# Performance work log

Measured on AMD Instinct MI355X. Metric: run time of the kernel, lower is better.

## Reference

```python
import jax, jax.numpy as jnp
import numpy as np

S, B, V, E, H, L, HM = 256, 16, 20000, 512, 256, 2, 128  # seq, batch, vocab, emb, hidden, layers, mlp hidden
THRESH = 0.5


def setup_inputs() -> dict:
    key = jax.random.key(0)
    ks = jax.random.split(key, 8)
    sc = 0.05
    concepts = jax.random.randint(ks[0], (S, B), 0, V)
    concepts_lengths = jnp.full((B,), S, dtype=jnp.int32)  # full-length sequences
    emb = jax.random.normal(ks[1], (V, E), jnp.float32) * sc
    # stacked PyTorch-style LSTM weights: [layer, direction(0=fwd,1=bwd), 4H, in]
    w_ih = jax.random.normal(ks[2], (L, 2, 4 * H, E), jnp.float32) * sc
    w_hh = jax.random.normal(ks[3], (L, 2, 4 * H, H), jnp.float32) * sc
    b = jax.random.normal(ks[4], (L, 2, 4 * H), jnp.float32) * sc  # b_ih + b_hh combined
    Ua = jax.random.normal(ks[5], (HM, 2 * H), jnp.float32) * sc
    Wa = jax.random.normal(ks[6], (HM, 2 * H), jnp.float32) * sc
    va = jax.random.normal(ks[7], (1, HM), jnp.float32) * sc
    return dict(concepts=concepts, concepts_lengths=concepts_lengths, emb=emb,
                w_ih=w_ih, w_hh=w_hh, b=b, Ua=Ua, Wa=Wa, va=va)


def _lstm_dir(x, wi, wh, bb, reverse):
    # x: [S, B, in]; PyTorch gate order i, f, g, o
    h0 = jnp.zeros((x.shape[1], H), x.dtype)

    def step(carry, xt):
        h, c = carry
        g = xt @ wi.T + h @ wh.T + bb  # [B, 4H]
        i, f, gg, o = jnp.split(g, 4, axis=-1)
        c = jax.nn.sigmoid(f) * c + jax.nn.sigmoid(i) * jnp.tanh(gg)
        h = jax.nn.sigmoid(o) * jnp.tanh(c)
        return (h, c), h

    _, hs = jax.lax.scan(step, (h0, h0), x, reverse=reverse)
    return hs  # [S, B, H]


def reference(concepts, concepts_lengths, emb, w_ih, w_hh, b, Ua, Wa, va):
    x = emb[concepts]  # [S, B, E]
    for l in range(L):  # fixed small layer count
        f = _lstm_dir(x, w_ih[l, 0], w_hh[l, 0], b[l, 0], False)
        r = _lstm_dir(x, w_ih[l, 1], w_hh[l, 1], b[l, 1], True)
        x = jnp.concatenate([f, r], axis=-1)  # [S, B, 2H]
    enc = x.transpose(1, 0, 2)  # [B, S, 2H]
    p = enc @ Ua.T  # [B, S, HM]  Ua(parent)
    c = enc @ Wa.T  # [B, S, HM]  Wa(child)
    # fused pairwise: va(tanh(Ua(p_i) + Wa(c_j))) -> [B, S, S]
    scores = jnp.einsum('bijh,h->bij', jnp.tanh(p[:, :, None, :] + c[:, None, :, :]), va[0])
    predictions = (jax.nn.sigmoid(scores) >= THRESH).astype(jnp.int32)
    return scores, predictions
```

## Files before the change

kernel.cpp:

```cpp
#include <hip/hip_runtime.h>


#define S_    256
#define B_    16
#define E_    512
#define H_    256
#define HM_   128
#define M_    4096

typedef __attribute__((ext_vector_type(8))) short short8;
typedef __attribute__((ext_vector_type(4))) float f32x4;
union u32x4s8 { unsigned int u[4]; uint4 u4; short8 v; };

__device__ __forceinline__ float sigm(float x) { return 1.f / (1.f + __expf(-x)); }
__device__ __forceinline__ float tanh_fast(float x) {
  x = fminf(fmaxf(x, -15.f), 15.f);
  float e = __expf(2.f * x);
  return (e - 1.f) / (e + 1.f);
}
__device__ __forceinline__ unsigned short f2bf(float f) {
  unsigned u = __float_as_uint(f);
  u += 0x7FFFu + ((u >> 16) & 1u);
  return (unsigned short)(u >> 16);
}
__device__ __forceinline__ float bf2f(unsigned short s) {
  return __uint_as_float(((unsigned)s) << 16);
}
__device__ __forceinline__ unsigned int packsplit(float f) {
  unsigned short m = f2bf(f);
  unsigned short r = f2bf(f - bf2f(m));
  return (unsigned)m | ((unsigned)r << 16);
}

__global__ void k_gather_pk(const int* __restrict__ concepts, const float* __restrict__ emb,
                            unsigned int* __restrict__ Xpk,
                            unsigned long long* __restrict__ hbz) {
  if (threadIdx.x < 8)
    hbz[(size_t)blockIdx.x * 8 + threadIdx.x] = 0ull;
  int m = blockIdx.x;
  int tok = concepts[m];
  const float4* src = reinterpret_cast<const float4*>(emb + (size_t)tok * E_);
  uint4* dst = reinterpret_cast<uint4*>(Xpk + (size_t)m * E_);
  for (int i = threadIdx.x; i < E_ / 4; i += blockDim.x) {
    float4 v = src[i];
    uint4 o;
    o.x = packsplit(v.x); o.y = packsplit(v.y); o.z = packsplit(v.z); o.w = packsplit(v.w);
    dst[i] = o;
  }
}

__global__ void k_pack(const float* __restrict__ in, unsigned int* __restrict__ out, int n4) {
  int i = blockIdx.x * blockDim.x + threadIdx.x;
  if (i < n4) {
    float4 v = reinterpret_cast<const float4*>(in)[i];
    uint4 o;
    o.x = packsplit(v.x); o.y = packsplit(v.y); o.z = packsplit(v.z); o.w = packsplit(v.w);
    reinterpret_cast<uint4*>(out)[i] = o;
  }
}

__global__ __launch_bounds__(256) void k_gemm_pk(const unsigned int* __restrict__ Apk,
                                                 const unsigned int* __restrict__ Wpk,
                                                 const float* __restrict__ bias,
                                                 float* __restrict__ C, int N, int K) {
  __shared__ unsigned int As[128][36];
  __shared__ unsigned int Ws2[128][36];
  const int bm = blockIdx.x * 128, bn = blockIdx.y * 128;
  const int tid = threadIdx.x;
  const int wave = tid >> 6, lane = tid & 63;
  const int wm = (wave >> 1) << 6, wn = (wave & 1) << 6;
  const int l16 = lane & 15, quad = lane >> 4;
  const int r = tid >> 1, cb = (tid & 1) << 4;

  f32x4 acc[4][4];
#pragma unroll
  for (int i = 0; i < 4; ++i)
#pragma unroll
    for (int j = 0; j < 4; ++j) acc[i][j] = (f32x4){0.f, 0.f, 0.f, 0.f};

  for (int k0 = 0; k0 < K; k0 += 32) {
    const unsigned int* pa = Apk + (size_t)(bm + r) * K + k0 + cb;
    const unsigned int* pw = Wpk + (size_t)(bn + r) * K + k0 + cb;
    uint4 a0 = *(const uint4*)pa, a1 = *(const uint4*)(pa + 4),
          a2 = *(const uint4*)(pa + 8), a3 = *(const uint4*)(pa + 12);
    uint4 w0 = *(const uint4*)pw, w1 = *(const uint4*)(pw + 4),
          w2 = *(const uint4*)(pw + 8), w3 = *(const uint4*)(pw + 12);
    __syncthreads();
    *(uint4*)&As[r][cb] = a0;  *(uint4*)&As[r][cb + 4] = a1;
    *(uint4*)&As[r][cb + 8] = a2; *(uint4*)&As[r][cb + 12] = a3;
    *(uint4*)&Ws2[r][cb] = w0; *(uint4*)&Ws2[r][cb + 4] = w1;
    *(uint4*)&Ws2[r][cb + 8] = w2; *(uint4*)&Ws2[r][cb + 12] = w3;
    __syncthreads();

    short8 Amv[4], Arv[4], Bmv[4], Brv[4];
#pragma unroll
    for (int t = 0; t < 4; ++t) {
      const unsigned int* p = &As[wm + (t << 4) + l16][quad << 3];
      uint4 p0 = *(const uint4*)p, p1 = *(const uint4*)(p + 4);
      u32x4s8 m, rr;
      m.u[0] = __builtin_amdgcn_perm(p0.y, p0.x, 0x05040100u);
      rr.u[0] = __builtin_amdgcn_perm(p0.y, p0.x, 0x07060302u);
      m.u[1] = __builtin_amdgcn_perm(p0.w, p0.z, 0x05040100u);
      rr.u[1] = __builtin_amdgcn_perm(p0.w, p0.z, 0x07060302u);
      m.u[2] = __builtin_amdgcn_perm(p1.y, p1.x, 0x05040100u);
      rr.u[2] = __builtin_amdgcn_perm(p1.y, p1.x, 0x07060302u);
      m.u[3] = __builtin_amdgcn_perm(p1.w, p1.z, 0x05040100u);
      rr.u[3] = __builtin_amdgcn_perm(p1.w, p1.z, 0x07060302u);
      Amv[t] = m.v; Arv[t] = rr.v;
      const unsigned int* pb = &Ws2[wn + (t << 4) + l16][quad << 3];
      uint4 q0 = *(const uint4*)pb, q1 = *(const uint4*)(pb + 4);
      m.u[0] = __builtin_amdgcn_perm(q0.y, q0.x, 0x05040100u);
      rr.u[0] = __builtin_amdgcn_perm(q0.y, q0.x, 0x07060302u);
      m.u[1] = __builtin_amdgcn_perm(q0.w, q0.z, 0x05040100u);
      rr.u[1] = __builtin_amdgcn_perm(q0.w, q0.z, 0x07060302u);
      m.u[2] = __builtin_amdgcn_perm(q1.y, q1.x, 0x05040100u);
      rr.u[2] = __builtin_amdgcn_perm(q1.y, q1.x, 0x07060302u);
      m.u[3] = __builtin_amdgcn_perm(q1.w, q1.z, 0x05040100u);
      rr.u[3] = __builtin_amdgcn_perm(q1.w, q1.z, 0x07060302u);
      Bmv[t] = m.v; Brv[t] = rr.v;
    }
#pragma unroll
    for (int ti = 0; ti < 4; ++ti)
#pragma unroll
      for (int tj = 0; tj < 4; ++tj) {
        acc[ti][tj] = __builtin_amdgcn_mfma_f32_16x16x32_bf16(Amv[ti], Bmv[tj], acc[ti][tj], 0, 0, 0);
        acc[ti][tj] = __builtin_amdgcn_mfma_f32_16x16x32_bf16(Amv[ti], Brv[tj], acc[ti][tj], 0, 0, 0);
        acc[ti][tj] = __builtin_amdgcn_mfma_f32_16x16x32_bf16(Arv[ti], Bmv[tj], acc[ti][tj], 0, 0, 0);
      }
  }

  float bv[4];
#pragma unroll
  for (int tj = 0; tj < 4; ++tj)
    bv[tj] = bias ? bias[bn + wn + (tj << 4) + l16] : 0.f;
#pragma unroll
  for (int ti = 0; ti < 4; ++ti)
#pragma unroll
    for (int rr = 0; rr < 4; ++rr) {
      float* crow = C + (size_t)(bm + wm + (ti << 4) + (quad << 2) + rr) * N + bn + wn + l16;
      crow[0]  = acc[ti][0][rr] + bv[0];
      crow[16] = acc[ti][1][rr] + bv[1];
      crow[32] = acc[ti][2][rr] + bv[2];
      crow[48] = acc[ti][3][rr] + bv[3];
    }
}

__global__ __launch_bounds__(256) void k_gemm2(const float* __restrict__ A,
                                               const float* __restrict__ W0,
                                               const float* __restrict__ W1,
                                               float* __restrict__ C0,
                                               float* __restrict__ C1,
                                               int N, int K) {
  __shared__ __align__(16) float As[16][132];
  __shared__ __align__(16) float Ws[16][132];
  const float* W = blockIdx.y ? W1 : W0;
  float* C = blockIdx.y ? C1 : C0;
  const int bm = blockIdx.x * 128;
  const int tid = threadIdx.x;
  const int tm = (tid >> 4) * 8, tn = (tid & 15) * 8;
  float acc[8][8];
#pragma unroll
  for (int i = 0; i < 8; i++)
#pragma unroll
    for (int j = 0; j < 8; j++) acc[i][j] = 0.f;

  const int lr = tid >> 1, lk = (tid & 1) * 8;
  for (int k0 = 0; k0 < K; k0 += 16) {
    float4 a0 = *(const float4*)(A + (size_t)(bm + lr) * K + k0 + lk);
    float4 a1 = *(const float4*)(A + (size_t)(bm + lr) * K + k0 + lk + 4);
    float4 w0 = *(const float4*)(W + (size_t)(lr) * K + k0 + lk);
    float4 w1 = *(const float4*)(W + (size_t)(lr) * K + k0 + lk + 4);
    As[lk + 0][lr] = a0.x; As[lk + 1][lr] = a0.y; As[lk + 2][lr] = a0.z; As[lk + 3][lr] = a0.w;
    As[lk + 4][lr] = a1.x; As[lk + 5][lr] = a1.y; As[lk + 6][lr] = a1.z; As[lk + 7][lr] = a1.w;
    Ws[lk + 0][lr] = w0.x; Ws[lk + 1][lr] = w0.y; Ws[lk + 2][lr] = w0.z; Ws[lk + 3][lr] = w0.w;
    Ws[lk + 4][lr] = w1.x; Ws[lk + 5][lr] = w1.y; Ws[lk + 6][lr] = w1.z; Ws[lk + 7][lr] = w1.w;
    __syncthreads();
#pragma unroll
    for (int k = 0; k < 16; k++) {
      float4 av0 = *(const float4*)&As[k][tm];
      float4 av1 = *(const float4*)&As[k][tm + 4];
      float4 wv0 = *(const float4*)&Ws[k][tn];
      float4 wv1 = *(const float4*)&Ws[k][tn + 4];
      float a[8] = {av0.x, av0.y, av0.z, av0.w, av1.x, av1.y, av1.z, av1.w};
      float w[8] = {wv0.x, wv0.y, wv0.z, wv0.w, wv1.x, wv1.y, wv1.z, wv1.w};
#pragma unroll
      for (int i = 0; i < 8; i++)
#pragma unroll
        for (int j = 0; j < 8; j++) acc[i][j] += a[i] * w[j];
    }
    __syncthreads();
  }

#pragma unroll
  for (int i = 0; i < 8; i++) {
    float4 v0 = make_float4(acc[i][0], acc[i][1], acc[i][2], acc[i][3]);
    float4 v1 = make_float4(acc[i][4], acc[i][5], acc[i][6], acc[i][7]);
    *(float4*)(C + (size_t)(bm + tm + i) * N + tn) = v0;
    *(float4*)(C + (size_t)(bm + tm + i) * N + tn + 4) = v1;
  }
}

__global__ __launch_bounds__(512) void k_lstm(const float* __restrict__ Gin,
                                              const float* __restrict__ whh,
                                              float* __restrict__ Houtf,
                                              unsigned int* __restrict__ Houtp,
                                              unsigned long long* __restrict__ Hbuf) {
  const int d = blockIdx.x >> 4;
  const int g = blockIdx.x & 15;
  const int tid = threadIdx.x;
  const int w8 = tid >> 6;
  const int lane = tid & 63;
  const int bcol = lane & 15;
  const int quad = lane >> 4;
  const int u_e = tid & 15;
  const int b_e = (tid >> 4) & 15;
  const int ws = (w8 + g) & 7;
  __shared__ unsigned int hL[16 * 260];
  __shared__ __align__(16) float Lg[4][16][24];

  unsigned int Am[8][4], Ar[8][4];
  if (w8 < 4) {
    const float* wrow = whh + (size_t)((d << 10) + (w8 << 8) + (g << 4) + bcol) * 256;
#pragma unroll
    for (int s = 0; s < 8; ++s) {
      float w[8];
      *(float4*)&w[0] = *(const float4*)(wrow + s * 32 + quad * 8);
      *(float4*)&w[4] = *(const float4*)(wrow + s * 32 + quad * 8 + 4);
#pragma unroll
      for (int j = 0; j < 4; ++j) {
        unsigned short m0 = f2bf(w[2 * j]), m1 = f2bf(w[2 * j + 1]);
        unsigned short r0 = f2bf(w[2 * j] - bf2f(m0));
        unsigned short r1 = f2bf(w[2 * j + 1] - bf2f(m1));
        Am[s][j] = (unsigned)m0 | ((unsigned)m1 << 16);
        Ar[s][j] = (unsigned)r0 | ((unsigned)r1 << 16);
      }
    }
  }

  float c_reg = 0.f;
  for (int it = 0; it < 256; ++it) {
    const int step = d ? (255 - it) : it;

    float gin[4];
    if (tid < 256) {
#pragma unroll
      for (int qq = 0; qq < 4; ++qq)
        gin[qq] = Gin[((size_t)((step << 4) + b_e) << 11) + (d << 10) + (qq << 8) + (g << 4) + u_e];
    }

    if (it > 0) {
      const unsigned long long* src = Hbuf + ((size_t)((d << 1) + ((it - 1) & 1)) << 12);
      const unsigned long long* p0 = src + (ws << 9) + lane;
      const unsigned int want = (unsigned int)it;
      unsigned long long v[8];
#pragma unroll
      for (int c = 0; c < 8; ++c)
        v[c] = __hip_atomic_load(p0 + (c << 6), __ATOMIC_RELAXED, __HIP_MEMORY_SCOPE_AGENT);
      for (;;) {
        unsigned int badm = 0;
#pragma unroll
        for (int c = 0; c < 8; ++c)
          badm |= ((unsigned int)(v[c] >> 32) != want) ? (1u << c) : 0u;
        if (__ballot(badm != 0) == 0ull) break;
#pragma unroll
        for (int c = 0; c < 8; ++c)
          if (badm & (1u << c))
            v[c] = __hip_atomic_load(p0 + (c << 6), __ATOMIC_RELAXED, __HIP_MEMORY_SCOPE_AGENT);
      }
#pragma unroll
      for (int c = 0; c < 8; ++c) {
        int e_b = (ws << 1) + (c >> 2);
        int e_k = ((c & 3) << 6) + lane;
        hL[e_b * 260 + e_k] = (unsigned int)v[c];
      }
    }
    __syncthreads();

    if (w8 < 4) {
      f32x4 acc0 = {0.f, 0.f, 0.f, 0.f}, acc1 = acc0, acc2 = acc0;
      if (it > 0) {
#pragma unroll
        for (int s = 0; s < 8; ++s) {
          const unsigned int* p = &hL[bcol * 260 + (s << 5) + (quad << 3)];
          uint4 p0v = *(const uint4*)p;
          uint4 p1v = *(const uint4*)(p + 4);
          u32x4s8 Bm, Br, Amu, Aru;
          Bm.u[0] = __builtin_amdgcn_perm(p0v.y, p0v.x, 0x05040100u);
          Br.u[0] = __builtin_amdgcn_perm(p0v.y, p0v.x, 0x07060302u);
          Bm.u[1] = __builtin_amdgcn_perm(p0v.w, p0v.z, 0x05040100u);
          Br.u[1] = __builtin_amdgcn_perm(p0v.w, p0v.z, 0x07060302u);
          Bm.u[2] = __builtin_amdgcn_perm(p1v.y, p1v.x, 0x05040100u);
          Br.u[2] = __builtin_amdgcn_perm(p1v.y, p1v.x, 0x07060302u);
          Bm.u[3] = __builtin_amdgcn_perm(p1v.w, p1v.z, 0x05040100u);
          Br.u[3] = __builtin_amdgcn_perm(p1v.w, p1v.z, 0x07060302u);
#pragma unroll
          for (int j = 0; j < 4; ++j) { Amu.u[j] = Am[s][j]; Aru.u[j] = Ar[s][j]; }
          acc0 = __builtin_amdgcn_mfma_f32_16x16x32_bf16(Amu.v, Bm.v, acc0, 0, 0, 0);
          acc1 = __builtin_amdgcn_mfma_f32_16x16x32_bf16(Amu.v, Br.v, acc1, 0, 0, 0);
          acc2 = __builtin_amdgcn_mfma_f32_16x16x32_bf16(Aru.v, Bm.v, acc2, 0, 0, 0);
        }
      }
      f32x4 t = acc0 + acc1 + acc2;
      *(float4*)&Lg[w8][bcol][quad << 2] = make_float4(t[0], t[1], t[2], t[3]);
    }
    __syncthreads();

    if (tid < 256) {
      float gi = Lg[0][b_e][u_e] + gin[0];
      float gf = Lg[1][b_e][u_e] + gin[1];
      float gg = Lg[2][b_e][u_e] + gin[2];
      float go = Lg[3][b_e][u_e] + gin[3];
      float ct = sigm(gf) * c_reg + sigm(gi) * tanh_fast(gg);
      c_reg = ct;
      float h = sigm(go) * tanh_fast(ct);
      unsigned short hm = f2bf(h);
      unsigned short hr = f2bf(h - bf2f(hm));
      unsigned int hpk = ((unsigned)hr << 16) | (unsigned)hm;
      unsigned long long hp = ((unsigned long long)(unsigned int)(it + 1) << 32) |
                              (unsigned long long)hpk;
      __hip_atomic_store(Hbuf + ((size_t)((d << 1) + (it & 1)) << 12) + (b_e << 8) + (g << 4) + u_e,
                         hp, __ATOMIC_RELAXED, __HIP_MEMORY_SCOPE_AGENT);
      size_t oidx = (size_t)((step << 4) + b_e) * 512 + (d << 8) + (g << 4) + u_e;
      Houtf[oidx] = h;
      Houtp[oidx] = hpk;
    }
  }
}

__global__ __launch_bounds__(256) void k_attn(const float* __restrict__ P,
                                              const float* __restrict__ Cc,
                                              const float* __restrict__ va,
                                              float* __restrict__ out) {
  const int b = blockIdx.x & 15, i = blockIdx.x >> 4;
  __shared__ float pv[128], vv[128];
  const int t = threadIdx.x;
  if (t < 128) {
    pv[t] = P[(size_t)((i << 4) + b) * 128 + t];
    vv[t] = va[t];
  }
  __syncthreads();
  const float4* c4 = reinterpret_cast<const float4*>(Cc + (size_t)((t << 4) + b) * 128);
  float acc = 0.f;
#pragma unroll 8
  for (int hh = 0; hh < 32; ++hh) {
    float4 cv = c4[hh];
    int h = hh << 2;
    acc += vv[h]     * tanh_fast(pv[h]     + cv.x);
    acc += vv[h + 1] * tanh_fast(pv[h + 1] + cv.y);
    acc += vv[h + 2] * tanh_fast(pv[h + 2] + cv.z);
    acc += vv[h + 3] * tanh_fast(pv[h + 3] + cv.w);
  }
  size_t o = ((size_t)b << 16) + ((size_t)i << 8) + (size_t)t;
  out[o] = acc;
  out[(1u << 20) + o] = (acc >= 0.f) ? 1.f : 0.f;
}

extern "C" void kernel_launch(void* const* d_in, const int* in_sizes, int n_in,
                              void* d_out, int out_size, void* d_ws, size_t ws_size,
                              hipStream_t stream) {
  const int*   concepts = (const int*)d_in[0];
  const float* emb  = (const float*)d_in[2];
  const float* w_ih = (const float*)d_in[3];
  const float* w_hh = (const float*)d_in[4];
  const float* bias = (const float*)d_in[5];
  const float* Ua   = (const float*)d_in[6];
  const float* Wa   = (const float*)d_in[7];
  const float* va   = (const float*)d_in[8];
  float* out = (float*)d_out;
  float* ws  = (float*)d_ws;

  constexpr size_t OFF_G   = 0;
  constexpr size_t OFF_PK  = OFF_G  + (size_t)M_ * 2048;
  constexpr size_t OFF_WPK = OFF_PK + (size_t)M_ * 512;
  constexpr size_t OFF_HF  = OFF_WPK + 2 * 2048 * 512;
  constexpr size_t OFF_P   = OFF_HF + (size_t)M_ * 512;
  constexpr size_t OFF_C   = OFF_P  + (size_t)M_ * HM_;
  constexpr size_t OFF_HB  = OFF_C  + (size_t)M_ * HM_;

  float* G  = ws + OFF_G;
  unsigned int* PK  = (unsigned int*)(ws + OFF_PK);
  unsigned int* WPK = (unsigned int*)(ws + OFF_WPK);
  float* HF = ws + OFF_HF;
  float* Pm = ws + OFF_P;
  float* Cm = ws + OFF_C;
  unsigned long long* Hb0 = (unsigned long long*)(ws + OFF_HB);
  unsigned long long* Hb1 = Hb0 + 2 * 2 * 4096;

  k_pack<<<(2 * 2048 * 512 / 4 + 255) / 256, 256, 0, stream>>>(w_ih, WPK, 2 * 2048 * 512 / 4);
  k_gather_pk<<<M_, 128, 0, stream>>>(concepts, emb, PK, Hb0);

  k_gemm_pk<<<dim3(32, 16), 256, 0, stream>>>(PK, WPK, bias, G, 2048, 512);
  k_lstm<<<32, 512, 0, stream>>>(G, w_hh, HF, PK, Hb0);

  k_gemm_pk<<<dim3(32, 16), 256, 0, stream>>>(PK, WPK + (size_t)2048 * 512, bias + 2048,
                                              G, 2048, 512);
  k_lstm<<<32, 512, 0, stream>>>(G, w_hh + (size_t)2048 * 256, HF, PK, Hb1);

  k_gemm2<<<dim3(32, 2), 256, 0, stream>>>(HF, Ua, Wa, Pm, Cm, HM_, 512);

  k_attn<<<M_, 256, 0, stream>>>(Pm, Cm, va, out);
}
```

Measured before the change: 1.491 ms.

## Interleave gate rows so MFMA output holds all four gates, drop shared-memory gate exchange

Reorders the recurrent weight rows each MFMA wave loads so that one lane's four accumulator outputs are the i, f, g, o gates for the same unit and batch. The LSTM cell update now runs directly from MFMA registers, which removes the Lg shared buffer and one __syncthreads per timestep. Polling of the previous hidden state moves to the four otherwise idle waves with a double-buffered shared tile so the compute and poll waves can overlap. Each poll wave now handles 16 loads instead of 8, and gate input loads shift onto the MFMA waves, which puts them on the critical path.

Result: slower. 2.147 ms (+44.0%).

```diff
diff --git a/kernel.cpp b/kernel.cpp
--- a/kernel.cpp
+++ b/kernel.cpp
@@ -212,15 +212,12 @@
   const int lane = tid & 63;
   const int bcol = lane & 15;
   const int quad = lane >> 4;
-  const int u_e = tid & 15;
-  const int b_e = (tid >> 4) & 15;
-  const int ws = (w8 + g) & 7;
-  __shared__ unsigned int hL[16 * 260];
-  __shared__ __align__(16) float Lg[4][16][24];
+  __shared__ unsigned int hL[2][16 * 260];
 
   unsigned int Am[8][4], Ar[8][4];
   if (w8 < 4) {
-    const float* wrow = whh + (size_t)((d << 10) + (w8 << 8) + (g << 4) + bcol) * 256;
+    const float* wrow = whh + (size_t)((d << 10) + ((bcol & 3) << 8) + (g << 4) +
+                                       (w8 << 2) + (bcol >> 2)) * 256;
 #pragma unroll
     for (int s = 0; s < 8; ++s) {
       float w[8];
@@ -236,52 +233,51 @@
       }
     }
   }
-
+  const int sw = w8 - 4;
   float c_reg = 0.f;
+
   for (int it = 0; it < 256; ++it) {
     const int step = d ? (255 - it) : it;
 
-    float gin[4];
-    if (tid < 256) {
-#pragma unroll
-      for (int qq = 0; qq < 4; ++qq)
-        gin[qq] = Gin[((size_t)((step << 4) + b_e) << 11) + (d << 10) + (qq << 8) + (g << 4) + u_e];
-    }
-
-    if (it > 0) {
+    if (w8 >= 4 && it > 0) {
       const unsigned long long* src = Hbuf + ((size_t)((d << 1) + ((it - 1) & 1)) << 12);
-      const unsigned long long* p0 = src + (ws << 9) + lane;
+      const unsigned long long* p0 = src + (sw << 6) + lane;
       const unsigned int want = (unsigned int)it;
-      unsigned long long v[8];
-#pragma unroll
-      for (int c = 0; c < 8; ++c)
-        v[c] = __hip_atomic_load(p0 + (c << 6), __ATOMIC_RELAXED, __HIP_MEMORY_SCOPE_AGENT);
+      unsigned long long v[16];
+#pragma unroll
+      for (int c = 0; c < 16; ++c)
+        v[c] = __hip_atomic_load(p0 + (c << 8), __ATOMIC_RELAXED, __HIP_MEMORY_SCOPE_AGENT);
       for (;;) {
         unsigned int badm = 0;
 #pragma unroll
-        for (int c = 0; c < 8; ++c)
+        for (int c = 0; c < 16; ++c)
           badm |= ((unsigned int)(v[c] >> 32) != want) ? (1u << c) : 0u;
         if (__ballot(badm != 0) == 0ull) break;
 #pragma unroll
-        for (int c = 0; c < 8; ++c)
+        for (int c = 0; c < 16; ++c)
           if (badm & (1u << c))
-            v[c] = __hip_atomic_load(p0 + (c << 6), __ATOMIC_RELAXED, __HIP_MEMORY_SCOPE_AGENT);
+            v[c] = __hip_atomic_load(p0 + (c << 8), __ATOMIC_RELAXED, __HIP_MEMORY_SCOPE_AGENT);
       }
-#pragma unroll
-      for (int c = 0; c < 8; ++c) {
-        int e_b = (ws << 1) + (c >> 2);
-        int e_k = ((c & 3) << 6) + lane;
-        hL[e_b * 260 + e_k] = (unsigned int)v[c];
-      }
+      unsigned int* hdst = &hL[it & 1][(sw << 6) + lane];
+#pragma unroll
+      for (int c = 0; c < 16; ++c)
+        hdst[c * 260] = (unsigned int)v[c];
     }
     __syncthreads();
 
     if (w8 < 4) {
+      float gin[4];
+#pragma unroll
+      for (int qq = 0; qq < 4; ++qq)
+        gin[qq] = Gin[((size_t)((step << 4) + bcol) << 11) + (d << 10) + (qq << 8) +
+                      (g << 4) + (w8 << 2) + quad];
+
       f32x4 acc0 = {0.f, 0.f, 0.f, 0.f}, acc1 = acc0, acc2 = acc0;
       if (it > 0) {
+        const unsigned int* hrow = &hL[it & 1][bcol * 260];
 #pragma unroll
         for (int s = 0; s < 8; ++s) {
-          const unsigned int* p = &hL[bcol * 260 + (s << 5) + (quad << 3)];
+          const unsigned int* p = hrow + (s << 5) + (quad << 3);
           uint4 p0v = *(const uint4*)p;
           uint4 p1v = *(const uint4*)(p + 4);
           u32x4s8 Bm, Br, Amu, Aru;
@@ -301,15 +297,11 @@
         }
       }
       f32x4 t = acc0 + acc1 + acc2;
-      *(float4*)&Lg[w8][bcol][quad << 2] = make_float4(t[0], t[1], t[2], t[3]);
-    }
-    __syncthreads();
-
-    if (tid < 256) {
-      float gi = Lg[0][b_e][u_e] + gin[0];
-      float gf = Lg[1][b_e][u_e] + gin[1];
-      float gg = Lg[2][b_e][u_e] + gin[2];
-      float go = Lg[3][b_e][u_e] + gin[3];
+
+      float gi = t[0] + gin[0];
+      float gf = t[1] + gin[1];
+      float gg = t[2] + gin[2];
+      float go = t[3] + gin[3];
       float ct = sigm(gf) * c_reg + sigm(gi) * tanh_fast(gg);
       c_reg = ct;
       float h = sigm(go) * tanh_fast(ct);
@@ -318,9 +310,11 @@
       unsigned int hpk = ((unsigned)hr << 16) | (unsigned)hm;
       unsigned long long hp = ((unsigned long long)(unsigned int)(it + 1) << 32) |
                               (unsigned long long)hpk;
-      __hip_atomic_store(Hbuf + ((size_t)((d << 1) + (it & 1)) << 12) + (b_e << 8) + (g << 4) + u_e,
+      __hip_atomic_store(Hbuf + ((size_t)((d << 1) + (it & 1)) << 12) +
+                         (bcol << 8) + (g << 4) + (w8 << 2) + quad,
                          hp, __ATOMIC_RELAXED, __HIP_MEMORY_SCOPE_AGENT);
-      size_t oidx = (size_t)((step << 4) + b_e) * 512 + (d << 8) + (g << 4) + u_e;
+      size_t oidx = (size_t)((step << 4) + bcol) * 512 + (d << 8) + (g << 4) +
+                    (w8 << 2) + quad;
       Houtf[oidx] = h;
       Houtp[oidx] = hpk;
     }
```
